# Kernel tuning notes

Measured on AMD Instinct MI355X. Metric: run time of the kernel, lower is better.

Reference implementation:

```python
import jax, jax.numpy as jnp
import numpy as np
import math

B, S, D, H = 2, 2048, 1024, 16
HD = D // H  # 64
BASE = 10000.0


def setup_inputs() -> dict:
    key = jax.random.key(0)
    ks = jax.random.split(key, 11)
    n = lambda k, shape, s=1.0: jax.random.normal(k, shape, dtype=jnp.float32) * s
    return {
        "q": n(ks[0], (B, S, D)),
        "k": n(ks[1], (B, S, D)),
        "v": n(ks[2], (B, S, D)),
        "Wq": n(ks[3], (D, D), 0.02), "bq": n(ks[4], (D,), 0.02),
        "Wk": n(ks[5], (D, D), 0.02), "bk": n(ks[6], (D,), 0.02),
        "Wv": n(ks[7], (D, D), 0.02), "bv": n(ks[8], (D,), 0.02),
        "Wo": n(ks[9], (D, D), 0.02), "bo": n(ks[10], (D,), 0.02),
    }


def _rope_tables():
    # theta: (HD/2,), angles: (S, HD/2)
    theta = 1.0 / (BASE ** (jnp.arange(0, HD, 2, dtype=jnp.float32) / HD))
    ang = jnp.arange(S, dtype=jnp.float32)[:, None] * theta[None, :]
    return jnp.cos(ang), jnp.sin(ang)


def _apply_rope(x, cos, sin):
    # x: (B, S, H, HD); rotate consecutive pairs along last dim
    xs = x.reshape(B, S, H, HD // 2, 2)
    c = cos[None, :, None, :]
    s = sin[None, :, None, :]
    r0 = xs[..., 0] * c - xs[..., 1] * s
    r1 = xs[..., 1] * c + xs[..., 0] * s
    return jnp.stack([r0, r1], axis=-1).reshape(B, S, H, HD)


def reference(q, k, v, Wq, bq, Wk, bk, Wv, bv, Wo, bo):
    act = lambda x: jax.nn.gelu(x, approximate=False)  # torch F.gelu (erf)
    qp = act(q @ Wq.T + bq)
    kp = act(k @ Wk.T + bk)
    vp = act(v @ Wv.T + bv)

    cos, sin = _rope_tables()
    qh = _apply_rope(qp.reshape(B, S, H, HD), cos, sin).reshape(B, S, D)
    kh = _apply_rope(kp.reshape(B, S, H, HD), cos, sin).reshape(B, S, D)

    # Faithful replication of original's raw view (B,S,D)->(S,B*H,HD)->transpose
    q2 = qh.reshape(S, B * H, HD).swapaxes(0, 1)  # (B*H, S, HD)
    k2 = kh.reshape(S, B * H, HD).swapaxes(0, 1)
    v2 = vp.reshape(S, B * H, HD).swapaxes(0, 1)

    scores = jnp.einsum('nqd,nkd->nqk', q2, k2) * math.sqrt(1.0 / float(D))
    weights = jax.nn.softmax(scores, axis=-1)  # dropout is identity in eval
    out = jnp.einsum('nqk,nkd->nqd', weights, v2)  # (B*H, S, HD)

    out = out.swapaxes(0, 1).reshape(S * B, D)
    out = act(out @ Wo.T + bo)
    return out.reshape(B, S, D)
```

## Files before the change

kernel.cpp:

```cpp
#include <hip/hip_runtime.h>
#include <hip/hip_bf16.h>
#include <stdint.h>

typedef __attribute__((ext_vector_type(4))) float f32x4;
typedef __attribute__((ext_vector_type(16))) float f32x16;
typedef __attribute__((ext_vector_type(8))) short short8;

#define DEV __device__ __forceinline__

DEV unsigned short f2bf(float f){
  unsigned u = __float_as_uint(f);
  u += 0x7FFFu + ((u >> 16) & 1u);
  return (unsigned short)(u >> 16);
}
DEV float erf_fast(float x){
  float ax = fabsf(x);
  float t = 1.0f / (1.0f + 0.3275911f * ax);
  float p = t * (0.254829592f + t * (-0.284496736f + t * (1.421413741f +
            t * (-1.453152027f + t * 1.061405429f))));
  float r = 1.0f - p * __expf(-ax * ax);
  return copysignf(r, x);
}
DEV float gelu_exact(float x){ return 0.5f * x * (1.0f + erf_fast(x * 0.70710678118654752f)); }

DEV void gl_lds16(const void* g, void* l){
  __builtin_amdgcn_global_load_lds((const __attribute__((address_space(1))) unsigned int*)g,
                                   (__attribute__((address_space(3))) unsigned int*)l, 16, 0, 0);
}

#define QSCALE 0.04508422f

struct ConvArgs { const float* src[7]; unsigned short* dst[7]; int n[7]; };

__global__ __launch_bounds__(256) void conv_kernel(ConvArgs a){
  int t = blockIdx.y;
  int i = (blockIdx.x * 256 + threadIdx.x) * 4;
  if (i >= a.n[t]) return;
  float4 v = *(const float4*)(a.src[t] + i);
  ushort4 o;
  o.x = f2bf(v.x); o.y = f2bf(v.y); o.z = f2bf(v.z); o.w = f2bf(v.w);
  *(ushort4*)(a.dst[t] + i) = o;
}

__global__ __launch_bounds__(256) void rope_kernel(float2* tab){
  int g = blockIdx.x * 256 + threadIdx.x;
  if (g >= 2048 * 32) return;
  int s = g >> 5, j = g & 31;
  float theta = (float)exp(-(double)j * (9.210340371976184 / 32.0));
  double ang = (double)s * (double)theta;
  tab[g] = make_float2((float)cos(ang), (float)sin(ang));
}

DEV void gemm_core128(const unsigned short* __restrict__ A, const unsigned short* __restrict__ W,
                      int m0, int n0, char* lds_raw, f32x4 (&acc)[4][4],
                      int lane, int wid, int wr, int wc)
{
  const int srow = wid * 8 + (lane >> 3);
  const int scc  = ((lane & 7) ^ (lane >> 3)) * 8;
  const int rxor = lane & 7;

  for (int kt = 0; kt < 16; ++kt){
    int kk = kt * 64;
    __syncthreads();
#pragma unroll
    for (int t = 0; t < 4; t++){
      gl_lds16(A + (size_t)(m0 + t * 32 + srow) * 1024 + kk + scc,
               lds_raw + (t * 2048 + wid * 512) * 2);
      gl_lds16(W + (size_t)(n0 + t * 32 + srow) * 1024 + kk + scc,
               lds_raw + 16384 + (t * 2048 + wid * 512) * 2);
    }
    __syncthreads();
    const unsigned short* Als = (const unsigned short*)lds_raw;
    const unsigned short* Bls = Als + 8192;
#pragma unroll
    for (int dk = 0; dk < 2; ++dk){
      short8 af[4], bfr[4];
      int cidx = (((dk * 4 + (lane >> 4)) ^ rxor) << 3);
#pragma unroll
      for (int i = 0; i < 4; i++){
        af[i]  = *(const short8*)(Als + (wr * 64 + i * 16 + (lane & 15)) * 64 + cidx);
        bfr[i] = *(const short8*)(Bls + (wc * 64 + i * 16 + (lane & 15)) * 64 + cidx);
      }
#pragma unroll
      for (int i = 0; i < 4; i++)
#pragma unroll
        for (int j = 0; j < 4; j++)
          acc[i][j] = __builtin_amdgcn_mfma_f32_16x16x32_bf16(af[i], bfr[j], acc[i][j], 0, 0, 0);
    }
  }
}

__global__ __launch_bounds__(256, 4)
void gemm_qkv(const unsigned short* __restrict__ Xq, const unsigned short* __restrict__ Xk, const unsigned short* __restrict__ Xv,
              const unsigned short* __restrict__ Wqb, const unsigned short* __restrict__ Wkb, const unsigned short* __restrict__ Wvb,
              const float* __restrict__ bq, const float* __restrict__ bk, const float* __restrict__ bv,
              unsigned short* __restrict__ Qg, unsigned short* __restrict__ Kg, unsigned short* __restrict__ Vtb,
              const float2* __restrict__ rtab)
{
  __shared__ __align__(16) char lds_raw[36864];
  const int z = blockIdx.z;
  const unsigned short* A = z == 0 ? Xq : z == 1 ? Xk : Xv;
  const unsigned short* W = z == 0 ? Wqb : z == 1 ? Wkb : Wvb;
  const float* bias = z == 0 ? bq : z == 1 ? bk : bv;
  unsigned short* outB = z == 0 ? Qg : z == 1 ? Kg : Vtb;

  const int tid = threadIdx.x, lane = tid & 63, wid = tid >> 6;
  const int wr = wid >> 1, wc = wid & 1;
  const int m0 = blockIdx.x * 128, n0 = blockIdx.y * 128;

  f32x4 acc[4][4];
#pragma unroll
  for (int i = 0; i < 4; i++)
#pragma unroll
    for (int j = 0; j < 4; j++)
#pragma unroll
      for (int r = 0; r < 4; r++) acc[i][j][r] = 0.0f;

  gemm_core128(A, W, m0, n0, lds_raw, acc, lane, wid, wr, wc);
  __syncthreads();

  if (z == 2){
    unsigned short* Tb = (unsigned short*)lds_raw + wid * 4608;
#pragma unroll
    for (int i = 0; i < 4; i++)
#pragma unroll
      for (int j = 0; j < 4; j++){
        int n = n0 + wc * 64 + j * 16 + (lane & 15);
        float b = bias[n];
#pragma unroll
        for (int r = 0; r < 4; r++){
          int il = i * 16 + (lane >> 4) * 4 + r;
          Tb[il * 72 + j * 16 + (lane & 15)] = f2bf(gelu_exact(acc[i][j][r] + b));
        }
      }
    __syncthreads();
    int mbase = m0 + wr * 64;
    int hh = (n0 + wc * 64) >> 6;
    int t = lane;
    int i0 = ((mbase >> 11) << 10) + ((mbase & 2047) >> 1);
#pragma unroll
    for (int p = 0; p < 2; p++){
      unsigned short* dst = outB + ((size_t)((hh + (p << 4)) * 64 + t)) * 2048 + i0;
#pragma unroll
      for (int g = 0; g < 8; g++){
        ushort4 pk;
        pk.x = Tb[(p + (g * 4 + 0) * 2) * 72 + t];
        pk.y = Tb[(p + (g * 4 + 1) * 2) * 72 + t];
        pk.z = Tb[(p + (g * 4 + 2) * 2) * 72 + t];
        pk.w = Tb[(p + (g * 4 + 3) * 2) * 72 + t];
        *(ushort4*)(dst + g * 4) = pk;
      }
    }
  } else {
    float scale = (z == 0) ? QSCALE : 1.0f;
#pragma unroll
    for (int i = 0; i < 4; i++)
#pragma unroll
      for (int j = 0; j < 4; j++){
        int n = n0 + wc * 64 + j * 16 + (lane & 15);
        float b = bias[n];
#pragma unroll
        for (int r = 0; r < 4; r++){
          int m = m0 + wr * 64 + i * 16 + (lane >> 4) * 4 + r;
          float val = gelu_exact(acc[i][j][r] + b);
          float pv = __shfl_xor(val, 1);
          int st = m & 2047;
          float2 cs = rtab[st * 32 + ((n >> 1) & 31)];
          float out = ((n & 1) == 0) ? (val * cs.x - pv * cs.y) : (val * cs.x + pv * cs.y);
          out *= scale;
          int nh = ((n >> 6) & 15) + ((st & 1) << 4);
          int ii = ((m >> 11) << 10) + (st >> 1);
          outB[(nh * 2048 + ii) * 64 + (n & 63)] = f2bf(out);
        }
      }
  }
}

__global__ __launch_bounds__(256, 4)
void gemm_o(const unsigned short* __restrict__ A, const unsigned short* __restrict__ W,
            const float* __restrict__ bias, float* __restrict__ outF)
{
  __shared__ __align__(16) char lds_raw[32768];
  const int tid = threadIdx.x, lane = tid & 63, wid = tid >> 6;
  const int wr = wid >> 1, wc = wid & 1;
  const int m0 = blockIdx.x * 128, n0 = blockIdx.y * 128;

  f32x4 acc[4][4];
#pragma unroll
  for (int i = 0; i < 4; i++)
#pragma unroll
    for (int j = 0; j < 4; j++)
#pragma unroll
      for (int r = 0; r < 4; r++) acc[i][j][r] = 0.0f;

  gemm_core128(A, W, m0, n0, lds_raw, acc, lane, wid, wr, wc);

#pragma unroll
  for (int i = 0; i < 4; i++)
#pragma unroll
    for (int j = 0; j < 4; j++){
      int n = n0 + wc * 64 + j * 16 + (lane & 15);
      float b = bias[n];
#pragma unroll
      for (int r = 0; r < 4; r++){
        int m = m0 + wr * 64 + i * 16 + (lane >> 4) * 4 + r;
        outF[m * 1024 + n] = gelu_exact(acc[i][j][r] + b);
      }
    }
}

__global__ __launch_bounds__(256)
void attn_kernel(const unsigned short* __restrict__ Qg,
                 const unsigned short* __restrict__ Kg,
                 const unsigned short* __restrict__ Vt,
                 unsigned short* __restrict__ attnO)
{
  __shared__ __align__(16) char lds_raw[16384];
  unsigned short* Kls = (unsigned short*)lds_raw;
  unsigned short* Vls = (unsigned short*)(lds_raw + 8192);
  const int tid = threadIdx.x, lane = tid & 63, wid = tid >> 6;
  const int q31 = lane & 31, h = lane >> 5;
  const int bid = blockIdx.x;
  const int n = (bid & 7) * 4 + ((bid >> 3) >> 4);
  const int qtile = (bid >> 3) & 15;
  const int qbase = qtile * 128;
  const unsigned short* Qn = Qg + (size_t)n * 2048 * 64;
  const unsigned short* Kn = Kg + (size_t)n * 2048 * 64;
  const unsigned short* Vn = Vt + (size_t)n * 64 * 2048;

  short8 qf[4];
  {
    int qrow = qbase + wid * 32 + q31;
#pragma unroll
    for (int c = 0; c < 4; c++)
      qf[c] = *(const short8*)(Qn + qrow * 64 + c * 16 + h * 8);
  }
  f32x16 o0, o1, lsum;
#pragma unroll
  for (int r = 0; r < 16; r++){ o0[r] = 0.0f; o1[r] = 0.0f; lsum[r] = 0.0f; }

  short8 rk[2], rv[2];
#pragma unroll
  for (int t = 0; t < 2; t++){
    int chunk = t * 256 + tid, row = chunk >> 3, c = chunk & 7;
    rk[t] = *(const short8*)(Kn + row * 64 + c * 8);
    rv[t] = *(const short8*)(Vn + row * 2048 + c * 8);
  }

  for (int kb = 0; kb < 2048; kb += 64){
    __syncthreads();
#pragma unroll
    for (int t = 0; t < 2; t++){
      int chunk = t * 256 + tid, row = chunk >> 3, c = chunk & 7;
      int sw = ((c ^ (row & 7)) << 3);
      *(short8*)(Kls + row * 64 + sw) = rk[t];
      *(short8*)(Vls + row * 64 + sw) = rv[t];
    }
    __syncthreads();
    if (kb + 64 < 2048){
#pragma unroll
      for (int t = 0; t < 2; t++){
        int chunk = t * 256 + tid, row = chunk >> 3, c = chunk & 7;
        rk[t] = *(const short8*)(Kn + (kb + 64 + row) * 64 + c * 8);
        rv[t] = *(const short8*)(Vn + row * 2048 + kb + 64 + c * 8);
      }
    }
    f32x16 s0, s1;
#pragma unroll
    for (int r = 0; r < 16; r++){ s0[r] = 0.0f; s1[r] = 0.0f; }
    __builtin_amdgcn_s_setprio(1);
#pragma unroll
    for (int c = 0; c < 4; c++){
      int sl = (c << 1) | h;
      short8 kf0 = *(const short8*)(Kls + q31 * 64 + ((sl ^ (q31 & 7)) << 3));
      s0 = __builtin_amdgcn_mfma_f32_32x32x16_bf16(kf0, qf[c], s0, 0, 0, 0);
      short8 kf1 = *(const short8*)(Kls + (32 + q31) * 64 + ((sl ^ (q31 & 7)) << 3));
      s1 = __builtin_amdgcn_mfma_f32_32x32x16_bf16(kf1, qf[c], s1, 0, 0, 0);
    }
    __builtin_amdgcn_s_setprio(0);
#pragma unroll
    for (int r = 0; r < 16; r++) s0[r] = exp2f(s0[r]);
#pragma unroll
    for (int r = 0; r < 16; r++) s1[r] = exp2f(s1[r]);
    lsum += s0;
    lsum += s1;
    __builtin_amdgcn_s_setprio(1);
#pragma unroll
    for (int kc = 0; kc < 4; kc++){
      const f32x16& S = (kc < 2) ? s0 : s1;
      const int rb = (kc & 1) * 8;
      unsigned a0, a1, b0, b1;
      asm("v_cvt_pk_bf16_f32 %0, %1, %2" : "=v"(a0) : "v"(S[rb + 0]), "v"(S[rb + 1]));
      asm("v_cvt_pk_bf16_f32 %0, %1, %2" : "=v"(a1) : "v"(S[rb + 2]), "v"(S[rb + 3]));
      asm("v_cvt_pk_bf16_f32 %0, %1, %2" : "=v"(b0) : "v"(S[rb + 4]), "v"(S[rb + 5]));
      asm("v_cvt_pk_bf16_f32 %0, %1, %2" : "=v"(b1) : "v"(S[rb + 6]), "v"(S[rb + 7]));
      asm("v_permlane32_swap_b32 %0, %1" : "+v"(a0), "+v"(b0));
      asm("v_permlane32_swap_b32 %0, %1" : "+v"(a1), "+v"(b1));
      union { int i[4]; short8 s; } u;
      u.i[0] = (int)a0; u.i[1] = (int)a1; u.i[2] = (int)b0; u.i[3] = (int)b1;
      short8 pf = u.s;
      int sl = (kc << 1) | h;
      {
        short8 vf = *(const short8*)(Vls + q31 * 64 + ((sl ^ (q31 & 7)) << 3));
        o0 = __builtin_amdgcn_mfma_f32_32x32x16_bf16(vf, pf, o0, 0, 0, 0);
      }
      {
        int dr = 32 + q31;
        short8 vf = *(const short8*)(Vls + dr * 64 + ((sl ^ (dr & 7)) << 3));
        o1 = __builtin_amdgcn_mfma_f32_32x32x16_bf16(vf, pf, o1, 0, 0, 0);
      }
    }
    __builtin_amdgcn_s_setprio(0);
  }
  float l = 0.0f;
#pragma unroll
  for (int r = 0; r < 16; r++) l += lsum[r];
  l += __shfl_xor(l, 32);
  float rl = 1.0f / l;
  const int p_par = n >> 4, head = n & 15;
  int ig = qbase + wid * 32 + q31;
  size_t rbase = ((size_t)(((ig >> 10) << 11) + ((ig & 1023) << 1) + p_par)) * 1024 + head * 64;
#pragma unroll
  for (int r = 0; r < 16; r++){
    int dl = (r & 3) + 8 * (r >> 2) + 4 * h;
    attnO[rbase + dl]      = f2bf(o0[r] * rl);
    attnO[rbase + 32 + dl] = f2bf(o1[r] * rl);
  }
}

extern "C" void kernel_launch(void* const* d_in, const int* in_sizes, int n_in,
                              void* d_out, int out_size, void* d_ws, size_t ws_size,
                              hipStream_t stream)
{
  const float* q  = (const float*)d_in[0];
  const float* k  = (const float*)d_in[1];
  const float* v  = (const float*)d_in[2];
  const float* Wq = (const float*)d_in[3];
  const float* bq = (const float*)d_in[4];
  const float* Wk = (const float*)d_in[5];
  const float* bk = (const float*)d_in[6];
  const float* Wv = (const float*)d_in[7];
  const float* bv = (const float*)d_in[8];
  const float* Wo = (const float*)d_in[9];
  const float* bo = (const float*)d_in[10];

  char* ws = (char*)d_ws;
  size_t off = 0;
  auto alloc = [&](size_t bytes) -> void* {
    void* p = ws + off;
    off += (bytes + 255) & ~(size_t)255;
    return p;
  };
  unsigned short* Xq  = (unsigned short*)alloc(4194304ull * 2);
  unsigned short* Xk  = (unsigned short*)alloc(4194304ull * 2);
  unsigned short* Xv  = (unsigned short*)alloc(4194304ull * 2);
  unsigned short* Wqb = (unsigned short*)alloc(1048576ull * 2);
  unsigned short* Wkb = (unsigned short*)alloc(1048576ull * 2);
  unsigned short* Wvb = (unsigned short*)alloc(1048576ull * 2);
  unsigned short* Wob = (unsigned short*)alloc(1048576ull * 2);
  unsigned short* Qg  = (unsigned short*)alloc(4194304ull * 2);
  unsigned short* Kg  = (unsigned short*)alloc(4194304ull * 2);
  unsigned short* Vtb = (unsigned short*)alloc(4194304ull * 2);
  unsigned short* aO  = (unsigned short*)alloc(4194304ull * 2);
  float2*         rtab = (float2*)alloc(2048ull * 32 * 8);

  ConvArgs ca;
  const float* srcs[7] = {q, k, v, Wq, Wk, Wv, Wo};
  unsigned short* dsts[7] = {Xq, Xk, Xv, Wqb, Wkb, Wvb, Wob};
  int ns[7] = {4194304, 4194304, 4194304, 1048576, 1048576, 1048576, 1048576};
  for (int i = 0; i < 7; i++){ ca.src[i] = srcs[i]; ca.dst[i] = dsts[i]; ca.n[i] = ns[i]; }

  conv_kernel<<<dim3(4096, 7), 256, 0, stream>>>(ca);
  rope_kernel<<<dim3(256), 256, 0, stream>>>(rtab);
  gemm_qkv<<<dim3(32, 8, 3), 256, 0, stream>>>(Xq, Xk, Xv, Wqb, Wkb, Wvb, bq, bk, bv, Qg, Kg, Vtb, rtab);
  attn_kernel<<<dim3(512), 256, 0, stream>>>(Qg, Kg, Vtb, aO);
  gemm_o<<<dim3(32, 8), 256, 0, stream>>>(aO, Wob, bo, (float*)d_out);
}
```

Before: 141.8 us.

## Load K and V fragments directly from global memory, dropping LDS staging

Removes the shared-memory staging of K and V tiles, the register prefetch and both block barriers per iteration. Each wave now loads its MFMA K and V fragments straight from global memory into registers before use. This drops the LDS write/read traffic and synchronisation, but every wave in a block now fetches the same K/V data separately, relying on L1/L2 to serve it. Load latency is also no longer hidden by the previous software prefetch.

```diff
diff --git a/kernel.cpp b/kernel.cpp
--- a/kernel.cpp
+++ b/kernel.cpp
@@ -215,9 +215,6 @@
                  const unsigned short* __restrict__ Vt,
                  unsigned short* __restrict__ attnO)
 {
-  __shared__ __align__(16) char lds_raw[16384];
-  unsigned short* Kls = (unsigned short*)lds_raw;
-  unsigned short* Vls = (unsigned short*)(lds_raw + 8192);
   const int tid = threadIdx.x, lane = tid & 63, wid = tid >> 6;
   const int q31 = lane & 31, h = lane >> 5;
   const int bid = blockIdx.x;
@@ -239,45 +236,36 @@
 #pragma unroll
   for (int r = 0; r < 16; r++){ o0[r] = 0.0f; o1[r] = 0.0f; lsum[r] = 0.0f; }
 
-  short8 rk[2], rv[2];
-#pragma unroll
-  for (int t = 0; t < 2; t++){
-    int chunk = t * 256 + tid, row = chunk >> 3, c = chunk & 7;
-    rk[t] = *(const short8*)(Kn + row * 64 + c * 8);
-    rv[t] = *(const short8*)(Vn + row * 2048 + c * 8);
-  }
+  const unsigned short* K0 = Kn + q31 * 64;
+  const unsigned short* K1 = Kn + (32 + q31) * 64;
+  const unsigned short* V0 = Vn + (size_t)q31 * 2048;
+  const unsigned short* V1 = Vn + (size_t)(32 + q31) * 2048;
 
   for (int kb = 0; kb < 2048; kb += 64){
-    __syncthreads();
-#pragma unroll
-    for (int t = 0; t < 2; t++){
-      int chunk = t * 256 + tid, row = chunk >> 3, c = chunk & 7;
-      int sw = ((c ^ (row & 7)) << 3);
-      *(short8*)(Kls + row * 64 + sw) = rk[t];
-      *(short8*)(Vls + row * 64 + sw) = rv[t];
-    }
-    __syncthreads();
-    if (kb + 64 < 2048){
-#pragma unroll
-      for (int t = 0; t < 2; t++){
-        int chunk = t * 256 + tid, row = chunk >> 3, c = chunk & 7;
-        rk[t] = *(const short8*)(Kn + (kb + 64 + row) * 64 + c * 8);
-        rv[t] = *(const short8*)(Vn + row * 2048 + kb + 64 + c * 8);
-      }
-    }
     f32x16 s0, s1;
 #pragma unroll
     for (int r = 0; r < 16; r++){ s0[r] = 0.0f; s1[r] = 0.0f; }
-    __builtin_amdgcn_s_setprio(1);
+    short8 kf0[4], kf1[4];
 #pragma unroll
     for (int c = 0; c < 4; c++){
       int sl = (c << 1) | h;
-      short8 kf0 = *(const short8*)(Kls + q31 * 64 + ((sl ^ (q31 & 7)) << 3));
-      s0 = __builtin_amdgcn_mfma_f32_32x32x16_bf16(kf0, qf[c], s0, 0, 0, 0);
-      short8 kf1 = *(const short8*)(Kls + (32 + q31) * 64 + ((sl ^ (q31 & 7)) << 3));
-      s1 = __builtin_amdgcn_mfma_f32_32x32x16_bf16(kf1, qf[c], s1, 0, 0, 0);
+      kf0[c] = *(const short8*)(K0 + kb * 64 + sl * 8);
+      kf1[c] = *(const short8*)(K1 + kb * 64 + sl * 8);
+    }
+    __builtin_amdgcn_s_setprio(1);
+#pragma unroll
+    for (int c = 0; c < 4; c++){
+      s0 = __builtin_amdgcn_mfma_f32_32x32x16_bf16(kf0[c], qf[c], s0, 0, 0, 0);
+      s1 = __builtin_amdgcn_mfma_f32_32x32x16_bf16(kf1[c], qf[c], s1, 0, 0, 0);
     }
     __builtin_amdgcn_s_setprio(0);
+    short8 vf0[4], vf1[4];
+#pragma unroll
+    for (int kc = 0; kc < 4; kc++){
+      int sl = (kc << 1) | h;
+      vf0[kc] = *(const short8*)(V0 + kb + sl * 8);
+      vf1[kc] = *(const short8*)(V1 + kb + sl * 8);
+    }
 #pragma unroll
     for (int r = 0; r < 16; r++) s0[r] = exp2f(s0[r]);
 #pragma unroll
@@ -299,16 +287,8 @@
       union { int i[4]; short8 s; } u;
       u.i[0] = (int)a0; u.i[1] = (int)a1; u.i[2] = (int)b0; u.i[3] = (int)b1;
       short8 pf = u.s;
-      int sl = (kc << 1) | h;
-      {
-        short8 vf = *(const short8*)(Vls + q31 * 64 + ((sl ^ (q31 & 7)) << 3));
-        o0 = __builtin_amdgcn_mfma_f32_32x32x16_bf16(vf, pf, o0, 0, 0, 0);
-      }
-      {
-        int dr = 32 + q31;
-        short8 vf = *(const short8*)(Vls + dr * 64 + ((sl ^ (dr & 7)) << 3));
-        o1 = __builtin_amdgcn_mfma_f32_32x32x16_bf16(vf, pf, o1, 0, 0, 0);
-      }
+      o0 = __builtin_amdgcn_mfma_f32_32x32x16_bf16(vf0[kc], pf, o0, 0, 0, 0);
+      o1 = __builtin_amdgcn_mfma_f32_32x32x16_bf16(vf1[kc], pf, o1, 0, 0, 0);
     }
     __builtin_amdgcn_s_setprio(0);
   }
```

After: 198.4 us. 39.9% more time.

## Split attention KV range across two blocks, fold output permutation into gemm_o loads

Applied to the files above, without the earlier changes.

The attention kernel now optionally splits the 2048-long KV range into two halves, so 1024 blocks run instead of 512. Each half writes unnormalized fp32 partial outputs and row sums, and a new norm kernel merges them into a head-major bf16 buffer. The row-sum is computed with an MFMA against a ones vector instead of vector adds, exp2 uses the hardware builtin, and gemm_o gathers its A tiles directly from the head-major layout, so the attention epilogue no longer does a scattered permuted store. The cost is an extra kernel launch and roughly 34 MB of fp32 partial traffic. The split path only runs if the workspace is large enough.

```diff
diff --git a/kernel.cpp b/kernel.cpp
--- a/kernel.cpp
+++ b/kernel.cpp
@@ -5,6 +5,7 @@
 typedef __attribute__((ext_vector_type(4))) float f32x4;
 typedef __attribute__((ext_vector_type(16))) float f32x16;
 typedef __attribute__((ext_vector_type(8))) short short8;
+typedef __attribute__((ext_vector_type(4))) short short4v;
 
 #define DEV __device__ __forceinline__
 
@@ -22,6 +23,14 @@
   return copysignf(r, x);
 }
 DEV float gelu_exact(float x){ return 0.5f * x * (1.0f + erf_fast(x * 0.70710678118654752f)); }
+
+DEV float exp2_fast(float x){
+#if __has_builtin(__builtin_amdgcn_exp2f)
+  return __builtin_amdgcn_exp2f(x);
+#else
+  return exp2f(x);
+#endif
+}
 
 DEV void gl_lds16(const void* g, void* l){
   __builtin_amdgcn_global_load_lds((const __attribute__((address_space(1))) unsigned int*)g,
@@ -177,7 +186,7 @@
 }
 
 __global__ __launch_bounds__(256, 4)
-void gemm_o(const unsigned short* __restrict__ A, const unsigned short* __restrict__ W,
+void gemm_o(const unsigned short* __restrict__ aOg, const unsigned short* __restrict__ W,
             const float* __restrict__ bias, float* __restrict__ outF)
 {
   __shared__ __align__(16) char lds_raw[32768];
@@ -193,8 +202,42 @@
 #pragma unroll
       for (int r = 0; r < 4; r++) acc[i][j][r] = 0.0f;
 
-  gemm_core128(A, W, m0, n0, lds_raw, acc, lane, wid, wr, wc);
-
+  const int srow = wid * 8 + (lane >> 3);
+  const int scc  = ((lane & 7) ^ (lane >> 3)) * 8;
+  const int rxor = lane & 7;
+
+  for (int kt = 0; kt < 16; ++kt){
+    int kk = kt * 64;
+    __syncthreads();
+#pragma unroll
+    for (int t = 0; t < 4; t++){
+      int row = m0 + t * 32 + srow;
+      int nn = kt + ((row & 1) << 4);
+      int iq = ((row >> 11) << 10) + ((row & 2047) >> 1);
+      gl_lds16(aOg + ((size_t)nn * 2048 + iq) * 64 + scc,
+               lds_raw + (t * 2048 + wid * 512) * 2);
+      gl_lds16(W + (size_t)(n0 + t * 32 + srow) * 1024 + kk + scc,
+               lds_raw + 16384 + (t * 2048 + wid * 512) * 2);
+    }
+    __syncthreads();
+    const unsigned short* Als = (const unsigned short*)lds_raw;
+    const unsigned short* Bls = Als + 8192;
+#pragma unroll
+    for (int dk = 0; dk < 2; ++dk){
+      short8 af[4], bfr[4];
+      int cidx = (((dk * 4 + (lane >> 4)) ^ rxor) << 3);
+#pragma unroll
+      for (int i = 0; i < 4; i++){
+        af[i]  = *(const short8*)(Als + (wr * 64 + i * 16 + (lane & 15)) * 64 + cidx);
+        bfr[i] = *(const short8*)(Bls + (wc * 64 + i * 16 + (lane & 15)) * 64 + cidx);
+      }
+#pragma unroll
+      for (int i = 0; i < 4; i++)
+#pragma unroll
+        for (int j = 0; j < 4; j++)
+          acc[i][j] = __builtin_amdgcn_mfma_f32_16x16x32_bf16(af[i], bfr[j], acc[i][j], 0, 0, 0);
+    }
+  }
 #pragma unroll
   for (int i = 0; i < 4; i++)
 #pragma unroll
@@ -209,11 +252,13 @@
     }
 }
 
-__global__ __launch_bounds__(256)
+template<int SPLIT>
+__global__ __launch_bounds__(256, 4)
 void attn_kernel(const unsigned short* __restrict__ Qg,
                  const unsigned short* __restrict__ Kg,
                  const unsigned short* __restrict__ Vt,
-                 unsigned short* __restrict__ attnO)
+                 unsigned short* __restrict__ aOg,
+                 float* __restrict__ Opart, float* __restrict__ Lpart)
 {
   __shared__ __align__(16) char lds_raw[16384];
   unsigned short* Kls = (unsigned short*)lds_raw;
@@ -221,9 +266,19 @@
   const int tid = threadIdx.x, lane = tid & 63, wid = tid >> 6;
   const int q31 = lane & 31, h = lane >> 5;
   const int bid = blockIdx.x;
-  const int n = (bid & 7) * 4 + ((bid >> 3) >> 4);
-  const int qtile = (bid >> 3) & 15;
+  int n, qtile, kvh;
+  if (SPLIT == 2){
+    int y = bid >> 3;
+    n = (bid & 7) * 4 + (y >> 5);
+    qtile = (y & 31) >> 1;
+    kvh = y & 1;
+  } else {
+    n = (bid & 7) * 4 + ((bid >> 3) >> 4);
+    qtile = (bid >> 3) & 15;
+    kvh = 0;
+  }
   const int qbase = qtile * 128;
+  const int kb0 = kvh * (2048 / SPLIT), kbN = kb0 + 2048 / SPLIT;
   const unsigned short* Qn = Qg + (size_t)n * 2048 * 64;
   const unsigned short* Kn = Kg + (size_t)n * 2048 * 64;
   const unsigned short* Vn = Vt + (size_t)n * 64 * 2048;
@@ -235,19 +290,23 @@
     for (int c = 0; c < 4; c++)
       qf[c] = *(const short8*)(Qn + qrow * 64 + c * 16 + h * 8);
   }
-  f32x16 o0, o1, lsum;
-#pragma unroll
-  for (int r = 0; r < 16; r++){ o0[r] = 0.0f; o1[r] = 0.0f; lsum[r] = 0.0f; }
+  short8 ones;
+#pragma unroll
+  for (int i = 0; i < 8; i++) ones[i] = (short)0x3F80;
+
+  f32x16 o0, o1, l_acc;
+#pragma unroll
+  for (int r = 0; r < 16; r++){ o0[r] = 0.0f; o1[r] = 0.0f; l_acc[r] = 0.0f; }
 
   short8 rk[2], rv[2];
 #pragma unroll
   for (int t = 0; t < 2; t++){
     int chunk = t * 256 + tid, row = chunk >> 3, c = chunk & 7;
-    rk[t] = *(const short8*)(Kn + row * 64 + c * 8);
-    rv[t] = *(const short8*)(Vn + row * 2048 + c * 8);
-  }
-
-  for (int kb = 0; kb < 2048; kb += 64){
+    rk[t] = *(const short8*)(Kn + (kb0 + row) * 64 + c * 8);
+    rv[t] = *(const short8*)(Vn + row * 2048 + kb0 + c * 8);
+  }
+
+  for (int kb = kb0; kb < kbN; kb += 64){
     __syncthreads();
 #pragma unroll
     for (int t = 0; t < 2; t++){
@@ -257,7 +316,7 @@
       *(short8*)(Vls + row * 64 + sw) = rv[t];
     }
     __syncthreads();
-    if (kb + 64 < 2048){
+    if (kb + 64 < kbN){
 #pragma unroll
       for (int t = 0; t < 2; t++){
         int chunk = t * 256 + tid, row = chunk >> 3, c = chunk & 7;
@@ -279,11 +338,9 @@
     }
     __builtin_amdgcn_s_setprio(0);
 #pragma unroll
-    for (int r = 0; r < 16; r++) s0[r] = exp2f(s0[r]);
-#pragma unroll
-    for (int r = 0; r < 16; r++) s1[r] = exp2f(s1[r]);
-    lsum += s0;
-    lsum += s1;
+    for (int r = 0; r < 16; r++) s0[r] = exp2_fast(s0[r]);
+#pragma unroll
+    for (int r = 0; r < 16; r++) s1[r] = exp2_fast(s1[r]);
     __builtin_amdgcn_s_setprio(1);
 #pragma unroll
     for (int kc = 0; kc < 4; kc++){
@@ -309,23 +366,58 @@
         short8 vf = *(const short8*)(Vls + dr * 64 + ((sl ^ (dr & 7)) << 3));
         o1 = __builtin_amdgcn_mfma_f32_32x32x16_bf16(vf, pf, o1, 0, 0, 0);
       }
+      l_acc = __builtin_amdgcn_mfma_f32_32x32x16_bf16(ones, pf, l_acc, 0, 0, 0);
     }
     __builtin_amdgcn_s_setprio(0);
   }
-  float l = 0.0f;
-#pragma unroll
-  for (int r = 0; r < 16; r++) l += lsum[r];
-  l += __shfl_xor(l, 32);
+
+  const float l = l_acc[0];
+  const int iq = qbase + wid * 32 + q31;
+
+  if (SPLIT == 2){
+    float* Ob = Opart + ((size_t)(kvh * 32 + n) * 64) * 2048;
+#pragma unroll
+    for (int r = 0; r < 16; r++){
+      int dl = (r & 3) + 8 * (r >> 2) + 4 * h;
+      Ob[(size_t)dl * 2048 + iq] = o0[r];
+      Ob[(size_t)(32 + dl) * 2048 + iq] = o1[r];
+    }
+    if (h == 0) Lpart[(size_t)(kvh * 32 + n) * 2048 + iq] = l;
+  } else {
+    float rl = 1.0f / l;
+    unsigned short* dst = aOg + ((size_t)n * 2048 + iq) * 64;
+#pragma unroll
+    for (int r = 0; r < 16; r++){
+      int dl = (r & 3) + 8 * (r >> 2) + 4 * h;
+      dst[dl]      = f2bf(o0[r] * rl);
+      dst[32 + dl] = f2bf(o1[r] * rl);
+    }
+  }
+}
+
+__global__ __launch_bounds__(256)
+void norm_kernel(const float* __restrict__ Opart, const float* __restrict__ Lpart,
+                 unsigned short* __restrict__ aOg)
+{
+  __shared__ unsigned short Tls[64 * 72];
+  const int n = blockIdx.x >> 5, iq0 = (blockIdx.x & 31) * 64;
+  const int tid = threadIdx.x;
+  const int iql = tid & 63, dg = tid >> 6;
+  float l = Lpart[(size_t)n * 2048 + iq0 + iql] + Lpart[(size_t)(32 + n) * 2048 + iq0 + iql];
   float rl = 1.0f / l;
-  const int p_par = n >> 4, head = n & 15;
-  int ig = qbase + wid * 32 + q31;
-  size_t rbase = ((size_t)(((ig >> 10) << 11) + ((ig & 1023) << 1) + p_par)) * 1024 + head * 64;
-#pragma unroll
-  for (int r = 0; r < 16; r++){
-    int dl = (r & 3) + 8 * (r >> 2) + 4 * h;
-    attnO[rbase + dl]      = f2bf(o0[r] * rl);
-    attnO[rbase + 32 + dl] = f2bf(o1[r] * rl);
-  }
+  const float* O0 = Opart + ((size_t)n * 64) * 2048;
+  const float* O1 = Opart + ((size_t)(32 + n) * 64) * 2048;
+#pragma unroll
+  for (int dd = 0; dd < 16; dd++){
+    int d = dg * 16 + dd;
+    float v = O0[(size_t)d * 2048 + iq0 + iql] + O1[(size_t)d * 2048 + iq0 + iql];
+    Tls[iql * 72 + d] = f2bf(v * rl);
+  }
+  __syncthreads();
+  const int iqr = tid >> 2, db = (tid & 3) * 16;
+  unsigned short* dst = aOg + ((size_t)n * 2048 + iq0 + iqr) * 64 + db;
+  *(short8*)(dst)     = *(const short8*)(Tls + iqr * 72 + db);
+  *(short8*)(dst + 8) = *(const short8*)(Tls + iqr * 72 + db + 8);
 }
 
 extern "C" void kernel_launch(void* const* d_in, const int* in_sizes, int n_in,
@@ -361,8 +453,11 @@
   unsigned short* Qg  = (unsigned short*)alloc(4194304ull * 2);
   unsigned short* Kg  = (unsigned short*)alloc(4194304ull * 2);
   unsigned short* Vtb = (unsigned short*)alloc(4194304ull * 2);
-  unsigned short* aO  = (unsigned short*)alloc(4194304ull * 2);
+  unsigned short* aOg = (unsigned short*)alloc(4194304ull * 2);
   float2*         rtab = (float2*)alloc(2048ull * 32 * 8);
+  float*          Opart = (float*)alloc(2ull * 32 * 64 * 2048 * 4);
+  float*          Lpart = (float*)alloc(2ull * 32 * 2048 * 4);
+  const bool split2 = (off <= ws_size);
 
   ConvArgs ca;
   const float* srcs[7] = {q, k, v, Wq, Wk, Wv, Wo};
@@ -373,6 +468,11 @@
   conv_kernel<<<dim3(4096, 7), 256, 0, stream>>>(ca);
   rope_kernel<<<dim3(256), 256, 0, stream>>>(rtab);
   gemm_qkv<<<dim3(32, 8, 3), 256, 0, stream>>>(Xq, Xk, Xv, Wqb, Wkb, Wvb, bq, bk, bv, Qg, Kg, Vtb, rtab);
-  attn_kernel<<<dim3(512), 256, 0, stream>>>(Qg, Kg, Vtb, aO);
-  gemm_o<<<dim3(32, 8), 256, 0, stream>>>(aO, Wob, bo, (float*)d_out);
-}
+  if (split2){
+    attn_kernel<2><<<dim3(1024), 256, 0, stream>>>(Qg, Kg, Vtb, aOg, Opart, Lpart);
+    norm_kernel<<<dim3(1024), 256, 0, stream>>>(Opart, Lpart, aOg);
+  } else {
+    attn_kernel<1><<<dim3(512), 256, 0, stream>>>(Qg, Kg, Vtb, aOg, nullptr, nullptr);
+  }
+  gemm_o<<<dim3(32, 8), 256, 0, stream>>>(aOg, Wob, bo, (float*)d_out);
+}
```

Result: slower. 169.1 us (+19.3%).

## Widen attention key tile to 128, fast exp2, head-major attn output gathered in gemm_o

Applied to the files above, without the earlier changes.

The attention kernel now stages 128 keys per iteration instead of 64, doubling LDS to 32KB. This halves the number of barrier and reload rounds and issues more MFMAs per sync. exp2 now uses the hardware builtin where available. The attention output is written in a contiguous head-major layout, and gemm_o gathers rows from that layout with its own global-to-LDS load loop rather than the shared gemm core. This removes the strided scattered stores in attention but makes the A-operand loads in gemm_o strided. Larger LDS and register use may lower occupancy.

```diff
diff --git a/kernel.cpp b/kernel.cpp
--- a/kernel.cpp
+++ b/kernel.cpp
@@ -22,6 +22,14 @@
   return copysignf(r, x);
 }
 DEV float gelu_exact(float x){ return 0.5f * x * (1.0f + erf_fast(x * 0.70710678118654752f)); }
+
+DEV float exp2_fast(float x){
+#if __has_builtin(__builtin_amdgcn_exp2f)
+  return __builtin_amdgcn_exp2f(x);
+#else
+  return exp2f(x);
+#endif
+}
 
 DEV void gl_lds16(const void* g, void* l){
   __builtin_amdgcn_global_load_lds((const __attribute__((address_space(1))) unsigned int*)g,
@@ -177,7 +185,7 @@
 }
 
 __global__ __launch_bounds__(256, 4)
-void gemm_o(const unsigned short* __restrict__ A, const unsigned short* __restrict__ W,
+void gemm_o(const unsigned short* __restrict__ aOg, const unsigned short* __restrict__ W,
             const float* __restrict__ bias, float* __restrict__ outF)
 {
   __shared__ __align__(16) char lds_raw[32768];
@@ -193,8 +201,42 @@
 #pragma unroll
       for (int r = 0; r < 4; r++) acc[i][j][r] = 0.0f;
 
-  gemm_core128(A, W, m0, n0, lds_raw, acc, lane, wid, wr, wc);
-
+  const int srow = wid * 8 + (lane >> 3);
+  const int scc  = ((lane & 7) ^ (lane >> 3)) * 8;
+  const int rxor = lane & 7;
+
+  for (int kt = 0; kt < 16; ++kt){
+    int kk = kt * 64;
+    __syncthreads();
+#pragma unroll
+    for (int t = 0; t < 4; t++){
+      int row = m0 + t * 32 + srow;
+      int nn = kt + ((row & 1) << 4);
+      int iq = ((row >> 11) << 10) + ((row & 2047) >> 1);
+      gl_lds16(aOg + ((size_t)nn * 2048 + iq) * 64 + scc,
+               lds_raw + (t * 2048 + wid * 512) * 2);
+      gl_lds16(W + (size_t)(n0 + t * 32 + srow) * 1024 + kk + scc,
+               lds_raw + 16384 + (t * 2048 + wid * 512) * 2);
+    }
+    __syncthreads();
+    const unsigned short* Als = (const unsigned short*)lds_raw;
+    const unsigned short* Bls = Als + 8192;
+#pragma unroll
+    for (int dk = 0; dk < 2; ++dk){
+      short8 af[4], bfr[4];
+      int cidx = (((dk * 4 + (lane >> 4)) ^ rxor) << 3);
+#pragma unroll
+      for (int i = 0; i < 4; i++){
+        af[i]  = *(const short8*)(Als + (wr * 64 + i * 16 + (lane & 15)) * 64 + cidx);
+        bfr[i] = *(const short8*)(Bls + (wc * 64 + i * 16 + (lane & 15)) * 64 + cidx);
+      }
+#pragma unroll
+      for (int i = 0; i < 4; i++)
+#pragma unroll
+        for (int j = 0; j < 4; j++)
+          acc[i][j] = __builtin_amdgcn_mfma_f32_16x16x32_bf16(af[i], bfr[j], acc[i][j], 0, 0, 0);
+    }
+  }
 #pragma unroll
   for (int i = 0; i < 4; i++)
 #pragma unroll
@@ -209,15 +251,15 @@
     }
 }
 
-__global__ __launch_bounds__(256)
+__global__ __launch_bounds__(256, 2)
 void attn_kernel(const unsigned short* __restrict__ Qg,
                  const unsigned short* __restrict__ Kg,
                  const unsigned short* __restrict__ Vt,
-                 unsigned short* __restrict__ attnO)
+                 unsigned short* __restrict__ aOg)
 {
-  __shared__ __align__(16) char lds_raw[16384];
+  __shared__ __align__(16) char lds_raw[32768];
   unsigned short* Kls = (unsigned short*)lds_raw;
-  unsigned short* Vls = (unsigned short*)(lds_raw + 8192);
+  unsigned short* Vls = (unsigned short*)(lds_raw + 16384);
   const int tid = threadIdx.x, lane = tid & 63, wid = tid >> 6;
   const int q31 = lane & 31, h = lane >> 5;
   const int bid = blockIdx.x;
@@ -239,55 +281,60 @@
 #pragma unroll
   for (int r = 0; r < 16; r++){ o0[r] = 0.0f; o1[r] = 0.0f; lsum[r] = 0.0f; }
 
-  short8 rk[2], rv[2];
-#pragma unroll
-  for (int t = 0; t < 2; t++){
-    int chunk = t * 256 + tid, row = chunk >> 3, c = chunk & 7;
-    rk[t] = *(const short8*)(Kn + row * 64 + c * 8);
-    rv[t] = *(const short8*)(Vn + row * 2048 + c * 8);
-  }
-
-  for (int kb = 0; kb < 2048; kb += 64){
-    __syncthreads();
-#pragma unroll
-    for (int t = 0; t < 2; t++){
-      int chunk = t * 256 + tid, row = chunk >> 3, c = chunk & 7;
-      int sw = ((c ^ (row & 7)) << 3);
-      *(short8*)(Kls + row * 64 + sw) = rk[t];
-      *(short8*)(Vls + row * 64 + sw) = rv[t];
-    }
-    __syncthreads();
-    if (kb + 64 < 2048){
-#pragma unroll
-      for (int t = 0; t < 2; t++){
-        int chunk = t * 256 + tid, row = chunk >> 3, c = chunk & 7;
-        rk[t] = *(const short8*)(Kn + (kb + 64 + row) * 64 + c * 8);
-        rv[t] = *(const short8*)(Vn + row * 2048 + kb + 64 + c * 8);
-      }
-    }
-    f32x16 s0, s1;
-#pragma unroll
-    for (int r = 0; r < 16; r++){ s0[r] = 0.0f; s1[r] = 0.0f; }
+  short8 rk[4], rv[4];
+#pragma unroll
+  for (int t = 0; t < 4; t++){
+    int chunk = t * 256 + tid;
+    rk[t] = *(const short8*)(Kn + (chunk >> 3) * 64 + (chunk & 7) * 8);
+    rv[t] = *(const short8*)(Vn + (size_t)(chunk >> 4) * 2048 + (chunk & 15) * 8);
+  }
+
+  for (int kb = 0; kb < 2048; kb += 128){
+    __syncthreads();
+#pragma unroll
+    for (int t = 0; t < 4; t++){
+      int chunk = t * 256 + tid;
+      { int row = chunk >> 3, c = chunk & 7;
+        *(short8*)(Kls + row * 64 + ((c ^ (row & 7)) << 3)) = rk[t]; }
+      { int row = chunk >> 4, c = chunk & 15;
+        *(short8*)(Vls + row * 128 + ((c ^ (row & 7)) << 3)) = rv[t]; }
+    }
+    __syncthreads();
+    if (kb + 128 < 2048){
+#pragma unroll
+      for (int t = 0; t < 4; t++){
+        int chunk = t * 256 + tid;
+        rk[t] = *(const short8*)(Kn + (kb + 128 + (chunk >> 3)) * 64 + (chunk & 7) * 8);
+        rv[t] = *(const short8*)(Vn + (size_t)(chunk >> 4) * 2048 + kb + 128 + (chunk & 15) * 8);
+      }
+    }
+    f32x16 s[4];
+#pragma unroll
+    for (int g = 0; g < 4; g++)
+#pragma unroll
+      for (int r = 0; r < 16; r++) s[g][r] = 0.0f;
     __builtin_amdgcn_s_setprio(1);
 #pragma unroll
     for (int c = 0; c < 4; c++){
       int sl = (c << 1) | h;
-      short8 kf0 = *(const short8*)(Kls + q31 * 64 + ((sl ^ (q31 & 7)) << 3));
-      s0 = __builtin_amdgcn_mfma_f32_32x32x16_bf16(kf0, qf[c], s0, 0, 0, 0);
-      short8 kf1 = *(const short8*)(Kls + (32 + q31) * 64 + ((sl ^ (q31 & 7)) << 3));
-      s1 = __builtin_amdgcn_mfma_f32_32x32x16_bf16(kf1, qf[c], s1, 0, 0, 0);
+#pragma unroll
+      for (int g = 0; g < 4; g++){
+        int row = g * 32 + q31;
+        short8 kf = *(const short8*)(Kls + row * 64 + ((sl ^ (row & 7)) << 3));
+        s[g] = __builtin_amdgcn_mfma_f32_32x32x16_bf16(kf, qf[c], s[g], 0, 0, 0);
+      }
     }
     __builtin_amdgcn_s_setprio(0);
 #pragma unroll
-    for (int r = 0; r < 16; r++) s0[r] = exp2f(s0[r]);
-#pragma unroll
-    for (int r = 0; r < 16; r++) s1[r] = exp2f(s1[r]);
-    lsum += s0;
-    lsum += s1;
+    for (int g = 0; g < 4; g++){
+#pragma unroll
+      for (int r = 0; r < 16; r++) s[g][r] = exp2_fast(s[g][r]);
+      lsum += s[g];
+    }
     __builtin_amdgcn_s_setprio(1);
 #pragma unroll
-    for (int kc = 0; kc < 4; kc++){
-      const f32x16& S = (kc < 2) ? s0 : s1;
+    for (int kc = 0; kc < 8; kc++){
+      const f32x16& S = s[kc >> 1];
       const int rb = (kc & 1) * 8;
       unsigned a0, a1, b0, b1;
       asm("v_cvt_pk_bf16_f32 %0, %1, %2" : "=v"(a0) : "v"(S[rb + 0]), "v"(S[rb + 1]));
@@ -301,12 +348,12 @@
       short8 pf = u.s;
       int sl = (kc << 1) | h;
       {
-        short8 vf = *(const short8*)(Vls + q31 * 64 + ((sl ^ (q31 & 7)) << 3));
+        short8 vf = *(const short8*)(Vls + q31 * 128 + ((sl ^ (q31 & 7)) << 3));
         o0 = __builtin_amdgcn_mfma_f32_32x32x16_bf16(vf, pf, o0, 0, 0, 0);
       }
       {
         int dr = 32 + q31;
-        short8 vf = *(const short8*)(Vls + dr * 64 + ((sl ^ (dr & 7)) << 3));
+        short8 vf = *(const short8*)(Vls + dr * 128 + ((sl ^ (dr & 7)) << 3));
         o1 = __builtin_amdgcn_mfma_f32_32x32x16_bf16(vf, pf, o1, 0, 0, 0);
       }
     }
@@ -317,14 +364,13 @@
   for (int r = 0; r < 16; r++) l += lsum[r];
   l += __shfl_xor(l, 32);
   float rl = 1.0f / l;
-  const int p_par = n >> 4, head = n & 15;
-  int ig = qbase + wid * 32 + q31;
-  size_t rbase = ((size_t)(((ig >> 10) << 11) + ((ig & 1023) << 1) + p_par)) * 1024 + head * 64;
+  const int iq = qbase + wid * 32 + q31;
+  unsigned short* dst = aOg + ((size_t)n * 2048 + iq) * 64;
 #pragma unroll
   for (int r = 0; r < 16; r++){
     int dl = (r & 3) + 8 * (r >> 2) + 4 * h;
-    attnO[rbase + dl]      = f2bf(o0[r] * rl);
-    attnO[rbase + 32 + dl] = f2bf(o1[r] * rl);
+    dst[dl]      = f2bf(o0[r] * rl);
+    dst[32 + dl] = f2bf(o1[r] * rl);
   }
 }
 
@@ -361,7 +407,7 @@
   unsigned short* Qg  = (unsigned short*)alloc(4194304ull * 2);
   unsigned short* Kg  = (unsigned short*)alloc(4194304ull * 2);
   unsigned short* Vtb = (unsigned short*)alloc(4194304ull * 2);
-  unsigned short* aO  = (unsigned short*)alloc(4194304ull * 2);
+  unsigned short* aOg = (unsigned short*)alloc(4194304ull * 2);
   float2*         rtab = (float2*)alloc(2048ull * 32 * 8);
 
   ConvArgs ca;
@@ -373,6 +419,6 @@
   conv_kernel<<<dim3(4096, 7), 256, 0, stream>>>(ca);
   rope_kernel<<<dim3(256), 256, 0, stream>>>(rtab);
   gemm_qkv<<<dim3(32, 8, 3), 256, 0, stream>>>(Xq, Xk, Xv, Wqb, Wkb, Wvb, bq, bk, bv, Qg, Kg, Vtb, rtab);
-  attn_kernel<<<dim3(512), 256, 0, stream>>>(Qg, Kg, Vtb, aO);
-  gemm_o<<<dim3(32, 8), 256, 0, stream>>>(aO, Wob, bo, (float*)d_out);
-}
+  attn_kernel<<<dim3(512), 256, 0, stream>>>(Qg, Kg, Vtb, aOg);
+  gemm_o<<<dim3(32, 8), 256, 0, stream>>>(aOg, Wob, bo, (float*)d_out);
+}
```

Measured after the change: 126.4 us. 10.9% less time.
